# Performance work log

Measured on AMD Instinct MI355X. Metric: run time of the kernel, lower is better.

Reference implementation:

```python
import jax, jax.numpy as jnp
import numpy as np

B, E, C, I, O, T = 8, 8, 1024, 128, 256, 8192

def setup_inputs() -> dict:
    key = jax.random.key(0)
    k1, k2, k3, k4, k5 = jax.random.split(key, 5)
    x_expert = jax.random.normal(k1, (B, E, C, I), dtype=jnp.float32)
    expert_indices = jax.random.randint(k2, (B, E, C), 0, T, dtype=jnp.int64 if jax.config.jax_enable_x64 else jnp.int32)
    expert_gate = jax.random.uniform(k3, (B, E, C), dtype=jnp.float32)
    # learned params: nn.Linear(in_features=1024, out_features=256) -> weight (O, in) viewed as (E, O, I)
    bound = 1.0 / np.sqrt(E * I)
    weight = jax.random.uniform(k4, (E, O, I), dtype=jnp.float32, minval=-bound, maxval=bound)
    bias = jax.random.uniform(k5, (O,), dtype=jnp.float32, minval=-bound, maxval=bound)
    return {"x_expert": x_expert, "expert_indices": expert_indices, "expert_gate": expert_gate,
            "weight": weight, "bias": bias, "num_tokens": T}

def reference(x_expert, expert_indices, expert_gate, weight, bias, num_tokens):
    # per-expert GEMM: (B,E,C,I) x (E,O,I) -> (B,E,C,O)
    y = jnp.einsum('beci,eoi->beco', x_expert, weight) + bias
    # gate scale: gate (B,E,C) -> (B,E,C,1)
    y = y * expert_gate[..., None]
    # scatter-add combine: flatten expert/capacity dims and index_add into (B, T, O)
    Bq, Eq, Cq, Oq = y.shape
    flat_y = y.reshape(Bq, Eq * Cq, Oq)
    flat_idx = expert_indices.reshape(Bq, Eq * Cq)
    out = jnp.zeros((Bq, num_tokens, Oq), dtype=y.dtype)
    batch_idx = jnp.arange(Bq)[:, None]  # (B,1) broadcasts against (B, E*C)
    out = out.at[batch_idx, flat_idx].add(flat_y)
    return out
```

## Files before the change

kernel.cpp:

```cpp
#include <hip/hip_runtime.h>

constexpr int Bn = 8;
constexpr int En = 8;
constexpr int Cn = 1024;
constexpr int In = 128;
constexpr int On = 256;
constexpr int Tn = 8192;
constexpr int ECn = En * Cn;

constexpr int TT  = 64;
constexpr int CAP = 16;
constexpr int OVF = 32;

typedef __fp16 fp16x2 __attribute__((ext_vector_type(2)));
typedef __fp16 f16x8  __attribute__((ext_vector_type(8)));
typedef float  f32x4  __attribute__((ext_vector_type(4)));

__device__ inline unsigned int pk16(float a, float b) {
    fp16x2 h = __builtin_amdgcn_cvt_pkrtz(a, b);
    return __builtin_bit_cast(unsigned int, h);
}

__global__ __launch_bounds__(256, 3)
void gemm_y(const float* __restrict__ x,
            const float* __restrict__ w,
            float* __restrict__ y)
{
    __shared__ uint4 Ah[TT * 16];

    const int tid = threadIdx.x;
    const int blk = blockIdx.x;
    const int b  = blk >> 7;
    const int e  = (blk >> 4) & 7;
    const int c0 = (blk & 15) * TT;

    const size_t becBase = ((size_t)(b * En + e)) * Cn + c0;
    const float* xrow = x + becBase * In;

    {
        const int tl = tid >> 2, cq = (tid & 3) * 4;
        const float4* xr = (const float4*)xrow + (size_t)tl * (In / 4);
        #pragma unroll
        for (int it = 0; it < 4; ++it) {
            int cc = cq + it;
            float4 a = xr[2 * cc], b2 = xr[2 * cc + 1];
            uint4 o;
            o.x = pk16(a.x, a.y);   o.y = pk16(a.z, a.w);
            o.z = pk16(b2.x, b2.y); o.w = pk16(b2.z, b2.w);
            Ah[tl * 16 + (cc ^ (tl & 15))] = o;
        }
    }

    const int l15  = tid & 15;
    const int q    = (tid >> 4) & 3;
    const int wcol = (tid >> 6) * 64;

    f16x8 bfr[4][4];
    #pragma unroll
    for (int nt = 0; nt < 4; ++nt)
        #pragma unroll
        for (int s = 0; s < 4; ++s) {
            const int col = wcol + 16 * nt + l15;
            const float4* p = (const float4*)w
                + ((size_t)(e * On + col)) * (In / 4) + (s * 8 + q * 2);
            float4 a = p[0], b2 = p[1];
            uint4 o;
            o.x = pk16(a.x, a.y);   o.y = pk16(a.z, a.w);
            o.z = pk16(b2.x, b2.y); o.w = pk16(b2.z, b2.w);
            bfr[nt][s] = __builtin_bit_cast(f16x8, o);
        }

    __syncthreads();

    f32x4 acc[4][4];
    #pragma unroll
    for (int mt = 0; mt < 4; ++mt)
        #pragma unroll
        for (int nt = 0; nt < 4; ++nt) acc[mt][nt] = f32x4{0.f, 0.f, 0.f, 0.f};

    #pragma unroll
    for (int mt = 0; mt < 4; ++mt) {
        const int tl = mt * 16 + l15;
        f16x8 afr[4];
        #pragma unroll
        for (int s = 0; s < 4; ++s)
            afr[s] = __builtin_bit_cast(f16x8, Ah[tl * 16 + ((4 * s + q) ^ (tl & 15))]);
        #pragma unroll
        for (int nt = 0; nt < 4; ++nt)
            #pragma unroll
            for (int s = 0; s < 4; ++s)
                acc[mt][nt] = __builtin_amdgcn_mfma_f32_16x16x32_f16(
                    afr[s], bfr[nt][s], acc[mt][nt], 0, 0, 0);
    }

    float* yb = y + becBase * On;
    #pragma unroll
    for (int mt = 0; mt < 4; ++mt) {
        #pragma unroll
        for (int i = 0; i < 4; ++i) {
            const int tl = mt * 16 + q * 4 + i;
            float* yr = yb + (size_t)tl * On + wcol + l15;
            #pragma unroll
            for (int nt = 0; nt < 4; ++nt)
                yr[16 * nt] = acc[mt][nt][i];
        }
    }
}

__global__ __launch_bounds__(256, 4)
void combine(const int*   __restrict__ idx,
             const float* __restrict__ gate,
             const float* __restrict__ y,
             const float* __restrict__ bias,
             float* __restrict__ out)
{
    __shared__ int   lcnt[TT];
    __shared__ float gsum[TT];
    __shared__ unsigned short lslot[TT][CAP];
    __shared__ float lgate[TT][CAP];
    __shared__ int ovfCnt;
    __shared__ unsigned ovfE[OVF];
    __shared__ float    ovfG[OVF];

    const int tid = threadIdx.x;
    const int blk = blockIdx.x;
    const int b  = blk >> 7;
    const int t0 = (blk & 127) * TT;
    const int*   idxb  = idx  + (size_t)b * ECn;
    const float* gateb = gate + (size_t)b * ECn;

    if (tid < TT) { lcnt[tid] = 0; gsum[tid] = 0.f; }
    if (tid == 0) ovfCnt = 0;
    __syncthreads();

    {
        const int4*   idx4  = (const int4*)idxb;
        const float4* gate4 = (const float4*)gateb;
        #pragma unroll
        for (int s = 0; s < ECn / 1024; ++s) {
            int i4 = tid + 256 * s;
            int4   tv = idx4[i4];
            float4 gv = gate4[i4];
            int ec0 = i4 * 4;
            #pragma unroll
            for (int k = 0; k < 4; ++k) {
                int   t = (k == 0) ? tv.x : (k == 1) ? tv.y : (k == 2) ? tv.z : tv.w;
                float g = (k == 0) ? gv.x : (k == 1) ? gv.y : (k == 2) ? gv.z : gv.w;
                unsigned d = (unsigned)(t - t0);
                if (d < (unsigned)TT) {
                    int ec = ec0 + k;
                    atomicAdd(&gsum[d], g);
                    int pos = atomicAdd(&lcnt[d], 1);
                    if (pos < CAP) {
                        lslot[d][pos] = (unsigned short)ec;
                        lgate[d][pos] = g;
                    } else {
                        int o = atomicAdd(&ovfCnt, 1);
                        if (o < OVF) { ovfE[o] = ((unsigned)d << 16) | (unsigned)ec; ovfG[o] = g; }
                    }
                }
            }
        }
    }
    __syncthreads();

    const int wv = tid >> 6;
    const int l  = tid & 63;
    const int d0 = wv * 16;
    const float* yb = y + (size_t)b * ECn * On;

    f32x4 acc[16];
    int   n[16];

    #pragma unroll
    for (int tk = 0; tk < 16; ++tk) {
        n[tk] = min(lcnt[d0 + tk], CAP);
        acc[tk] = f32x4{0.f, 0.f, 0.f, 0.f};
        if (n[tk] > 0) {
            const int ec = lslot[d0 + tk][0];
            acc[tk] = ((const f32x4*)(yb + (size_t)ec * On))[l];
        }
    }
    #pragma unroll
    for (int tk = 0; tk < 16; ++tk)
        if (n[tk] > 0) acc[tk] *= lgate[d0 + tk][0];

    #pragma unroll
    for (int tk = 0; tk < 16; ++tk) {
        for (int j = 1; j < n[tk]; ++j) {
            const int ec = lslot[d0 + tk][j];
            const float g = lgate[d0 + tk][j];
            f32x4 v = ((const f32x4*)(yb + (size_t)ec * On))[l];
            acc[tk] += v * g;
        }
    }

    const int oc = min(ovfCnt, OVF);
    for (int j = 0; j < oc; ++j) {
        const int dd = (int)(ovfE[j] >> 16);
        const int tk = dd - d0;
        if ((unsigned)tk < 16u) {
            const int ec = (int)(ovfE[j] & 0xFFFFu);
            const float g = ovfG[j];
            f32x4 v = ((const f32x4*)(yb + (size_t)ec * On))[l];
            #pragma unroll
            for (int k = 0; k < 16; ++k)
                if (tk == k) acc[k] += v * g;
        }
    }

    const f32x4 bv = ((const f32x4*)bias)[l];
    #pragma unroll
    for (int tk = 0; tk < 16; ++tk) {
        const int d = d0 + tk;
        const float gs = gsum[d];
        f32x4 r = acc[tk] + bv * gs;
        ((f32x4*)(out + ((size_t)b * Tn + t0 + d) * On))[l] = r;
    }
}

__global__ void prep_w(const float4* __restrict__ w4, uint4* __restrict__ wh4) {
    int f = blockIdx.x * 256 + threadIdx.x;
    int col = f & 255, q = (f >> 8) & 3, s = (f >> 10) & 3, e = f >> 12;
    const float4* p = w4 + ((size_t)(e * On + col)) * (In / 4) + (s * 8 + q * 2);
    float4 a = p[0], b = p[1];
    uint4 o;
    o.x = pk16(a.x, a.y); o.y = pk16(a.z, a.w);
    o.z = pk16(b.x, b.y); o.w = pk16(b.z, b.w);
    wh4[f] = o;
}

__global__ __launch_bounds__(256, 2)
void gemm_scatter(const float* __restrict__ x, const int* __restrict__ idx,
                  const float* __restrict__ gate, const uint4* __restrict__ wh4,
                  const float* __restrict__ bias, float* __restrict__ out)
{
    __shared__ uint4 Ah[TT * 16];
    __shared__ int   sIdx[TT];
    __shared__ float sG[TT];

    const int tid = threadIdx.x;
    const int blk = blockIdx.x;
    const int b  = blk >> 7;
    const int e  = (blk >> 4) & 7;
    const int c0 = (blk & 15) * TT;

    const size_t becBase = ((size_t)(b * En + e)) * Cn + c0;
    const float* xrow = x + becBase * In;

    if (tid < TT) {
        sIdx[tid] = idx[becBase + tid];
        sG[tid]   = gate[becBase + tid];
    }
    {
        const int tl = tid >> 2, cq = (tid & 3) * 4;
        const float4* xr = (const float4*)xrow + (size_t)tl * (In / 4);
        #pragma unroll
        for (int it = 0; it < 4; ++it) {
            int cc = cq + it;
            float4 a = xr[2 * cc], b2 = xr[2 * cc + 1];
            uint4 o;
            o.x = pk16(a.x, a.y);   o.y = pk16(a.z, a.w);
            o.z = pk16(b2.x, b2.y); o.w = pk16(b2.z, b2.w);
            Ah[tl * 16 + (cc ^ (tl & 15))] = o;
        }
    }
    const int l15  = tid & 15;
    const int q    = (tid >> 4) & 3;
    const int wcol = (tid >> 6) * 64;

    f16x8 bfr[4][4];
    #pragma unroll
    for (int nt = 0; nt < 4; ++nt)
        #pragma unroll
        for (int s = 0; s < 4; ++s)
            bfr[nt][s] = __builtin_bit_cast(f16x8,
                wh4[(size_t)((e * 4 + s) * 4 + q) * 256 + wcol + 16 * nt + l15]);

    __syncthreads();

    f32x4 acc[4][4];
    #pragma unroll
    for (int mt = 0; mt < 4; ++mt)
        #pragma unroll
        for (int nt = 0; nt < 4; ++nt) acc[mt][nt] = f32x4{0.f, 0.f, 0.f, 0.f};

    #pragma unroll
    for (int mt = 0; mt < 4; ++mt) {
        const int tl = mt * 16 + l15;
        f16x8 afr[4];
        #pragma unroll
        for (int s = 0; s < 4; ++s)
            afr[s] = __builtin_bit_cast(f16x8, Ah[tl * 16 + ((4 * s + q) ^ (tl & 15))]);
        #pragma unroll
        for (int nt = 0; nt < 4; ++nt)
            #pragma unroll
            for (int s = 0; s < 4; ++s)
                acc[mt][nt] = __builtin_amdgcn_mfma_f32_16x16x32_f16(
                    afr[s], bfr[nt][s], acc[mt][nt], 0, 0, 0);
    }

    float bv[4];
    #pragma unroll
    for (int nt = 0; nt < 4; ++nt) bv[nt] = bias[wcol + 16 * nt + l15];

    float* ob = out + (size_t)b * Tn * On;
    #pragma unroll
    for (int mt = 0; mt < 4; ++mt) {
        #pragma unroll
        for (int i = 0; i < 4; ++i) {
            const int tl = mt * 16 + q * 4 + i;
            const int t  = sIdx[tl];
            const float g = sG[tl];
            float* orow = ob + (size_t)t * On + wcol + l15;
            #pragma unroll
            for (int nt = 0; nt < 4; ++nt)
                atomicAdd(&orow[16 * nt], (acc[mt][nt][i] + bv[nt]) * g);
        }
    }
}

extern "C" void kernel_launch(void* const* d_in, const int* in_sizes, int n_in,
                              void* d_out, int out_size, void* d_ws, size_t ws_size,
                              hipStream_t stream) {
    const float* x    = (const float*)d_in[0];
    const int*   idx  = (const int*)  d_in[1];
    const float* gate = (const float*)d_in[2];
    const float* w    = (const float*)d_in[3];
    const float* bias = (const float*)d_in[4];
    float* out = (float*)d_out;

    const size_t needY = (size_t)Bn * ECn * On * sizeof(float);

    if (ws_size >= needY) {
        float* yws = (float*)d_ws;
        gemm_y <<<Bn * En * (Cn / TT), 256, 0, stream>>>(x, w, yws);
        combine<<<Bn * (Tn / TT),      256, 0, stream>>>(idx, gate, yws, bias, out);
    } else {
        uint4* wh4 = (uint4*)d_ws;
        prep_w<<<(En * 4 * 4 * On) / 256, 256, 0, stream>>>((const float4*)w, wh4);
        hipMemsetAsync(d_out, 0, (size_t)out_size, stream);
        gemm_scatter<<<Bn * En * (Cn / TT), 256, 0, stream>>>(x, idx, gate, wh4, bias, out);
    }
}
```

Measured before the change: 137.1 us.

## Store intermediate GEMM output in fp16 and prepack weights once

The intermediate y buffer written by the GEMM and read by the combine kernel is now stored as fp16 instead of fp32, which halves that round-trip traffic. The GEMM writes each lane's four output columns as one packed 8-byte store, and the combine kernel converts back to fp32 and writes the strided column layout that matches. Weights are pre-converted to fp16 fragments once by prep_w rather than converted in every GEMM block. This adds a kernel launch and loses precision in y, since rounding happens before the gate multiply and accumulation.

Measured after the change: 124.7 us. 9.1% less time.

```diff
diff --git a/kernel.cpp b/kernel.cpp
--- a/kernel.cpp
+++ b/kernel.cpp
@@ -20,11 +20,31 @@
     fp16x2 h = __builtin_amdgcn_cvt_pkrtz(a, b);
     return __builtin_bit_cast(unsigned int, h);
 }
+__device__ inline unsigned int pkrtn(float a, float b) {
+    fp16x2 h = { (__fp16)a, (__fp16)b };
+    return __builtin_bit_cast(unsigned int, h);
+}
+__device__ inline f32x4 yconv(uint2 r) {
+    fp16x2 a = __builtin_bit_cast(fp16x2, r.x);
+    fp16x2 b = __builtin_bit_cast(fp16x2, r.y);
+    return f32x4{(float)a.x, (float)a.y, (float)b.x, (float)b.y};
+}
+
+__global__ void prep_w(const float4* __restrict__ w4, uint4* __restrict__ wh4) {
+    int f = blockIdx.x * 256 + threadIdx.x;
+    int col = f & 255, q = (f >> 8) & 3, s = (f >> 10) & 3, e = f >> 12;
+    const float4* p = w4 + ((size_t)(e * On + col)) * (In / 4) + (s * 8 + q * 2);
+    float4 a = p[0], b = p[1];
+    uint4 o;
+    o.x = pk16(a.x, a.y); o.y = pk16(a.z, a.w);
+    o.z = pk16(b.x, b.y); o.w = pk16(b.z, b.w);
+    wh4[f] = o;
+}
 
 __global__ __launch_bounds__(256, 3)
 void gemm_y(const float* __restrict__ x,
-            const float* __restrict__ w,
-            float* __restrict__ y)
+            const uint4* __restrict__ wh4,
+            __fp16* __restrict__ y)
 {
     __shared__ uint4 Ah[TT * 16];
 
@@ -59,16 +79,9 @@
     #pragma unroll
     for (int nt = 0; nt < 4; ++nt)
         #pragma unroll
-        for (int s = 0; s < 4; ++s) {
-            const int col = wcol + 16 * nt + l15;
-            const float4* p = (const float4*)w
-                + ((size_t)(e * On + col)) * (In / 4) + (s * 8 + q * 2);
-            float4 a = p[0], b2 = p[1];
-            uint4 o;
-            o.x = pk16(a.x, a.y);   o.y = pk16(a.z, a.w);
-            o.z = pk16(b2.x, b2.y); o.w = pk16(b2.z, b2.w);
-            bfr[nt][s] = __builtin_bit_cast(f16x8, o);
-        }
+        for (int s = 0; s < 4; ++s)
+            bfr[nt][s] = __builtin_bit_cast(f16x8,
+                wh4[(size_t)((e * 4 + s) * 4 + q) * 256 + wcol + 16 * nt + l15]);
 
     __syncthreads();
 
@@ -93,16 +106,16 @@
                     afr[s], bfr[nt][s], acc[mt][nt], 0, 0, 0);
     }
 
-    float* yb = y + becBase * On;
+    __fp16* yb = y + becBase * On;
     #pragma unroll
     for (int mt = 0; mt < 4; ++mt) {
         #pragma unroll
         for (int i = 0; i < 4; ++i) {
             const int tl = mt * 16 + q * 4 + i;
-            float* yr = yb + (size_t)tl * On + wcol + l15;
-            #pragma unroll
-            for (int nt = 0; nt < 4; ++nt)
-                yr[16 * nt] = acc[mt][nt][i];
+            uint2 o;
+            o.x = pkrtn(acc[mt][0][i], acc[mt][1][i]);
+            o.y = pkrtn(acc[mt][2][i], acc[mt][3][i]);
+            *(uint2*)(yb + (size_t)tl * On + wcol + 4 * l15) = o;
         }
     }
 }
@@ -110,7 +123,7 @@
 __global__ __launch_bounds__(256, 4)
 void combine(const int*   __restrict__ idx,
              const float* __restrict__ gate,
-             const float* __restrict__ y,
+             const __fp16* __restrict__ y,
              const float* __restrict__ bias,
              float* __restrict__ out)
 {
@@ -167,30 +180,33 @@
     const int wv = tid >> 6;
     const int l  = tid & 63;
     const int d0 = wv * 16;
-    const float* yb = y + (size_t)b * ECn * On;
+    const __fp16* yb = y + (size_t)b * ECn * On;
 
     f32x4 acc[16];
     int   n[16];
 
+    uint2 raw[16];
     #pragma unroll
     for (int tk = 0; tk < 16; ++tk) {
         n[tk] = min(lcnt[d0 + tk], CAP);
-        acc[tk] = f32x4{0.f, 0.f, 0.f, 0.f};
+        raw[tk] = uint2{0u, 0u};
         if (n[tk] > 0) {
             const int ec = lslot[d0 + tk][0];
-            acc[tk] = ((const f32x4*)(yb + (size_t)ec * On))[l];
-        }
-    }
-    #pragma unroll
-    for (int tk = 0; tk < 16; ++tk)
-        if (n[tk] > 0) acc[tk] *= lgate[d0 + tk][0];
+            raw[tk] = *(const uint2*)(yb + (size_t)ec * On + 4 * l);
+        }
+    }
+    #pragma unroll
+    for (int tk = 0; tk < 16; ++tk) {
+        acc[tk] = f32x4{0.f, 0.f, 0.f, 0.f};
+        if (n[tk] > 0) acc[tk] = yconv(raw[tk]) * lgate[d0 + tk][0];
+    }
 
     #pragma unroll
     for (int tk = 0; tk < 16; ++tk) {
         for (int j = 1; j < n[tk]; ++j) {
             const int ec = lslot[d0 + tk][j];
             const float g = lgate[d0 + tk][j];
-            f32x4 v = ((const f32x4*)(yb + (size_t)ec * On))[l];
+            f32x4 v = yconv(*(const uint2*)(yb + (size_t)ec * On + 4 * l));
             acc[tk] += v * g;
         }
     }
@@ -202,32 +218,26 @@
         if ((unsigned)tk < 16u) {
             const int ec = (int)(ovfE[j] & 0xFFFFu);
             const float g = ovfG[j];
-            f32x4 v = ((const f32x4*)(yb + (size_t)ec * On))[l];
+            f32x4 v = yconv(*(const uint2*)(yb + (size_t)ec * On + 4 * l));
             #pragma unroll
             for (int k = 0; k < 16; ++k)
                 if (tk == k) acc[k] += v * g;
         }
     }
 
-    const f32x4 bv = ((const f32x4*)bias)[l];
+    const int cbase = (l >> 4) * 64 + (l & 15);
+    const float bv0 = bias[cbase],      bv1 = bias[cbase + 16];
+    const float bv2 = bias[cbase + 32], bv3 = bias[cbase + 48];
     #pragma unroll
     for (int tk = 0; tk < 16; ++tk) {
         const int d = d0 + tk;
         const float gs = gsum[d];
-        f32x4 r = acc[tk] + bv * gs;
-        ((f32x4*)(out + ((size_t)b * Tn + t0 + d) * On))[l] = r;
-    }
-}
-
-__global__ void prep_w(const float4* __restrict__ w4, uint4* __restrict__ wh4) {
-    int f = blockIdx.x * 256 + threadIdx.x;
-    int col = f & 255, q = (f >> 8) & 3, s = (f >> 10) & 3, e = f >> 12;
-    const float4* p = w4 + ((size_t)(e * On + col)) * (In / 4) + (s * 8 + q * 2);
-    float4 a = p[0], b = p[1];
-    uint4 o;
-    o.x = pk16(a.x, a.y); o.y = pk16(a.z, a.w);
-    o.z = pk16(b.x, b.y); o.w = pk16(b.z, b.w);
-    wh4[f] = o;
+        float* orow = out + ((size_t)b * Tn + t0 + d) * On + cbase;
+        orow[0]  = acc[tk][0] + bv0 * gs;
+        orow[16] = acc[tk][1] + bv1 * gs;
+        orow[32] = acc[tk][2] + bv2 * gs;
+        orow[48] = acc[tk][3] + bv3 * gs;
+    }
 }
 
 __global__ __launch_bounds__(256, 2)
@@ -330,15 +340,17 @@
     const float* bias = (const float*)d_in[4];
     float* out = (float*)d_out;
 
-    const size_t needY = (size_t)Bn * ECn * On * sizeof(float);
-
-    if (ws_size >= needY) {
-        float* yws = (float*)d_ws;
-        gemm_y <<<Bn * En * (Cn / TT), 256, 0, stream>>>(x, w, yws);
+    const size_t whBytes = 1u << 20;
+    const size_t needWs  = whBytes + (size_t)Bn * ECn * On * 2;
+
+    uint4* wh4 = (uint4*)d_ws;
+    prep_w<<<(En * 4 * 4 * On) / 256, 256, 0, stream>>>((const float4*)w, wh4);
+
+    if (ws_size >= needWs) {
+        __fp16* yws = (__fp16*)((char*)d_ws + whBytes);
+        gemm_y <<<Bn * En * (Cn / TT), 256, 0, stream>>>(x, wh4, yws);
         combine<<<Bn * (Tn / TT),      256, 0, stream>>>(idx, gate, yws, bias, out);
     } else {
-        uint4* wh4 = (uint4*)d_ws;
-        prep_w<<<(En * 4 * 4 * On) / 256, 256, 0, stream>>>((const float4*)w, wh4);
         hipMemsetAsync(d_out, 0, (size_t)out_size, stream);
         gemm_scatter<<<Bn * En * (Cn / TT), 256, 0, stream>>>(x, idx, gate, wh4, bias, out);
     }
```
